# Optimization experiments

Hardware: AMD Instinct MI355X
Metric: run time of the kernel (lower is better)

## Reference

```python
import jax, jax.numpy as jnp
import numpy as np
import math

K = 3
IN_CH = 512
OUT_CH = 512
W_DIM = 512
B = 16
HW = 64
LR_MUL = 1.0


def setup_inputs() -> dict:
    key = jax.random.key(0)
    k1, k2, k3, k4 = jax.random.split(key, 4)
    x = jax.random.normal(k1, (B, HW, HW, IN_CH), dtype=jnp.float32)
    w_latents = jax.random.normal(k2, (B, W_DIM), dtype=jnp.float32)
    w = jax.random.normal(k3, (K, K, IN_CH, OUT_CH), dtype=jnp.float32)  # init_std = 1/lr_mul = 1
    b = jnp.zeros((OUT_CH,), dtype=jnp.float32)
    fc_w = jax.random.normal(k4, (W_DIM, IN_CH), dtype=jnp.float32)
    fc_b = jnp.zeros((IN_CH,), dtype=jnp.float32)
    return {"x": x, "w_latents": w_latents, "w": w, "b": b, "fc_w": fc_w, "fc_b": fc_b}


def reference(x, w_latents, w, b, fc_w, fc_b):
    # equalized-LR runtime coefficients (gain=1)
    conv_coef = LR_MUL / math.sqrt(K * K * IN_CH)
    fc_coef = LR_MUL / math.sqrt(W_DIM)

    batch, H, W_, Cin = x.shape
    x_nchw = jnp.transpose(x, (0, 3, 1, 2))  # [B, Cin, H, W]

    weight = w * conv_coef  # [k,k,in,out]
    # style modulation: fully_connected (no lrelu) + 1
    s = w_latents @ (fc_w * fc_coef) + fc_b * LR_MUL + 1.0  # [B, in]

    # per-sample modulated weights [B,k,k,in,out]
    ww = weight[None] * s[:, None, None, :, None]
    # demodulation
    d = jax.lax.rsqrt(jnp.sum(jnp.square(ww), axis=(1, 2, 3)) + 1e-8)  # [B, out]
    ww = ww * d[:, None, None, None, :]

    # fused_modconv: grouped conv with groups = batch
    x_g = x_nchw.reshape(1, batch * Cin, H, W_)
    w_g = jnp.transpose(ww, (1, 2, 3, 0, 4)).reshape(K, K, Cin, batch * OUT_CH)
    y = jax.lax.conv_general_dilated(
        x_g, w_g,
        window_strides=(1, 1),
        padding='SAME',
        dimension_numbers=('NCHW', 'HWIO', 'NCHW'),
        feature_group_count=batch,
    )  # [1, B*out, H, W]
    y = y.reshape(batch, OUT_CH, H, W_)
    y = jnp.transpose(y, (0, 2, 3, 1))  # NHWC
    y = y + (b * LR_MUL)
    return y
```

## Files before the change

kernel.cpp:

```cpp
#include <hip/hip_runtime.h>
#include <hip/hip_bf16.h>

#define IN_CH 512
#define OUT_CH 512
#define W_DIM 512
#define BATCH 16
#define HWDIM 64
#define PADW 66

static constexpr float CONV_COEF = 0.014731391274719739f;
static constexpr float FC_COEF   = 0.044194173824159216f;

typedef __bf16 bf16x8 __attribute__((ext_vector_type(8)));
typedef float  f32x4  __attribute__((ext_vector_type(4)));

typedef __attribute__((address_space(1))) void gvoid;
typedef __attribute__((address_space(3))) void lvoid;

__device__ __forceinline__ void async_cp16(const void* g, void* l) {
    __builtin_amdgcn_global_load_lds((gvoid*)g, (lvoid*)l, 16, 0, 0);
}

__device__ __forceinline__ ushort f2bf(float f) {
    union { float f; unsigned u; } un; un.f = f;
    unsigned u = un.u;
    return (ushort)((u + 0x7fffu + ((u >> 16) & 1u)) >> 16);
}

__global__ void k_halo(ushort* __restrict__ xs) {
    int b = blockIdx.y;
    int pidx = blockIdx.x * 4 + (threadIdx.x >> 6);
    int ch = threadIdx.x & 63;
    int h, w;
    if (pidx < 66)       { h = 0;          w = pidx; }
    else if (pidx < 132) { h = 65;         w = pidx - 66; }
    else if (pidx < 196) { h = pidx - 131; w = 0; }
    else                 { h = pidx - 195; w = 65; }
    size_t base = (((size_t)(b * PADW + h)) * PADW + w) * IN_CH + ch * 8;
    uint4 z = {0u, 0u, 0u, 0u};
    *(uint4*)(xs + base) = z;
}

__global__ void k_style(const float* __restrict__ wl, const float* __restrict__ fcw,
                        const float* __restrict__ fcb, float* __restrict__ s) {
    int b = blockIdx.x;
    int i = blockIdx.y * 128 + threadIdx.x;
    __shared__ float lw[W_DIM];
    for (int j = threadIdx.x; j < W_DIM; j += 128) lw[j] = wl[b * W_DIM + j];
    __syncthreads();
    float acc = 0.f;
#pragma unroll 8
    for (int j = 0; j < W_DIM; ++j) acc += lw[j] * fcw[(size_t)j * IN_CH + i];
    s[b * IN_CH + i] = acc * FC_COEF + fcb[i] + 1.0f;
}

__global__ void k_xs(const float* __restrict__ x, const float* __restrict__ s,
                     ushort* __restrict__ xs) {
    int t = blockIdx.x * blockDim.x + threadIdx.x;
    int pix = t >> 7;
    int c = (t & 127) << 2;
    int b = pix >> 12;
    int hw = pix & 4095;
    int h = hw >> 6, w = hw & 63;
    float4 xv = ((const float4*)x)[t];
    float4 sv = ((const float4*)(s + b * IN_CH))[t & 127];
    ushort4 o;
    o.x = f2bf(xv.x * sv.x);
    o.y = f2bf(xv.y * sv.y);
    o.z = f2bf(xv.z * sv.z);
    o.w = f2bf(xv.w * sv.w);
    size_t dst = (((size_t)(b * PADW + h + 1)) * PADW + (w + 1)) * IN_CH + c;
    *(ushort4*)(xs + dst) = o;
}

__global__ void k_wt(const float* __restrict__ w, ushort* __restrict__ wT) {
    __shared__ float tile[32][33];
    int kk = blockIdx.z;
    const float* src = w + (size_t)kk * IN_CH * OUT_CH;
    ushort* dst = wT + (size_t)kk * IN_CH * OUT_CH;
    int i0 = blockIdx.y * 32;
    int o0 = blockIdx.x * 32;
    int tx = threadIdx.x, ty = threadIdx.y;
#pragma unroll
    for (int rr = 0; rr < 32; rr += 8)
        tile[ty + rr][tx] = src[(size_t)(i0 + ty + rr) * OUT_CH + o0 + tx];
    __syncthreads();
#pragma unroll
    for (int rr = 0; rr < 32; rr += 8)
        dst[(size_t)(o0 + ty + rr) * IN_CH + i0 + tx] = f2bf(tile[tx][ty + rr]);
}

__global__ void k_a2(const float* __restrict__ w, float* __restrict__ a2) {
    int n = blockIdx.x * blockDim.x + threadIdx.x;
    float sum = 0.f;
#pragma unroll
    for (int kk = 0; kk < 9; ++kk) {
        float v = w[(size_t)kk * (IN_CH * OUT_CH) + n];
        sum += v * v;
    }
    a2[n] = sum;
}

__global__ void k_dmod(const float* __restrict__ s, const float* __restrict__ a2,
                       float* __restrict__ dmod) {
    int b = blockIdx.x;
    int o = blockIdx.y * 128 + threadIdx.x;
    __shared__ float s2[IN_CH];
    for (int i = threadIdx.x; i < IN_CH; i += 128) {
        float v = s[b * IN_CH + i];
        s2[i] = v * v;
    }
    __syncthreads();
    float acc = 0.f;
#pragma unroll 8
    for (int i = 0; i < IN_CH; ++i) acc += s2[i] * a2[(size_t)i * OUT_CH + o];
    dmod[b * OUT_CH + o] = rsqrtf(acc * CONV_COEF * CONV_COEF + 1e-8f);
}


__device__ __forceinline__ int aoff_of(int t) {
    int kk = t >> 3;
    int c0 = (t & 7) << 6;
    int kh = (kk >= 6) ? 2 : ((kk >= 3) ? 1 : 0);
    int kw = kk - kh * 3;
    return (kh * PADW + kw) * IN_CH + c0;
}

__device__ __forceinline__ int boff_of(int t) {
    int kk = t >> 3;
    int c0 = (t & 7) << 6;
    return kk * (IN_CH * OUT_CH) + c0;
}

__device__ __forceinline__ void bar() {
    asm volatile("" ::: "memory");
    __builtin_amdgcn_s_barrier();
    asm volatile("" ::: "memory");
}

#define MFMA16(AV, MH)                                                        \
    __builtin_amdgcn_s_setprio(1);                                            \
    _Pragma("unroll")                                                         \
    for (int i = 0; i < 4; ++i)                                               \
        _Pragma("unroll")                                                     \
        for (int j = 0; j < 4; ++j)                                           \
            acc[(MH)*4 + i][j] = __builtin_amdgcn_mfma_f32_16x16x32_bf16(     \
                AV[i], bv[j], acc[(MH)*4 + i][j], 0, 0, 0);                   \
    __builtin_amdgcn_s_setprio(0);

__device__ __forceinline__ void step4(
    const ushort* __restrict__ aBase, const ushort* __restrict__ bBase,
    int pc0, int pc1,
    const ushort* __restrict__ gA, const ushort* __restrict__ gB,
    ushort* __restrict__ dA, ushort* __restrict__ dB,
    bool doStage, f32x4 (&acc)[8][4])
{
    bf16x8 av[4], bv[4];

#pragma unroll
    for (int f = 0; f < 4; ++f) bv[f] = *(const bf16x8*)(bBase + f * 1024 + pc0);
#pragma unroll
    for (int f = 0; f < 4; ++f) av[f] = *(const bf16x8*)(aBase + f * 1024 + pc0);
    if (doStage) {
#pragma unroll
        for (int i = 0; i < 4; ++i)
            async_cp16(gA + i * (PADW * IN_CH), dA + i * 4096);
    }
    bar();
    MFMA16(av, 0)
    bar();

#pragma unroll
    for (int f = 0; f < 4; ++f) av[f] = *(const bf16x8*)(aBase + 4096 + f * 1024 + pc0);
    if (doStage) {
#pragma unroll
        for (int i = 0; i < 4; ++i)
            async_cp16(gB + i * (64 * IN_CH), dB + i * 4096);
    }
    bar();
    MFMA16(av, 1)
    bar();

#pragma unroll
    for (int f = 0; f < 4; ++f) bv[f] = *(const bf16x8*)(bBase + f * 1024 + pc1);
#pragma unroll
    for (int f = 0; f < 4; ++f) av[f] = *(const bf16x8*)(aBase + f * 1024 + pc1);
    bar();
    MFMA16(av, 0)
    bar();

#pragma unroll
    for (int f = 0; f < 4; ++f) av[f] = *(const bf16x8*)(aBase + 4096 + f * 1024 + pc1);
    bar();
    MFMA16(av, 1)
    asm volatile("s_waitcnt vmcnt(0)" ::: "memory");
    bar();
}

__global__ __launch_bounds__(512, 2) void k_conv(
    const ushort* __restrict__ xs, const ushort* __restrict__ wT,
    const float* __restrict__ dmod, const float* __restrict__ bias,
    float* __restrict__ out) {
    __shared__ __align__(16) ushort smem[4][16384];

    const int tid = threadIdx.x;
    const int wave = tid >> 6;
    const int lane = tid & 63;
    const int srow = tid >> 3;
    const int lc = (tid & 7) ^ (srow & 7);

    const int wg = (blockIdx.x & 7) * 64 + (blockIdx.x >> 3);
    const int nt = wg >> 8;
    const int mt = wg & 255;
    const int b  = mt >> 4;
    const int h0 = (mt & 15) << 2;
    const int n0 = nt << 8;

    const ushort* gA0 = xs + (((size_t)(b * PADW + h0)) * PADW + srow) * IN_CH + lc * 8;
    const ushort* gB0 = wT + ((size_t)(n0 + srow)) * IN_CH + lc * 8;

    ushort* dA[2] = { &smem[0][wave * 512], &smem[2][wave * 512] };
    ushort* dB[2] = { &smem[1][wave * 512], &smem[3][wave * 512] };

    const int rlane = lane & 15;
    const int q = lane >> 4;
    const int wm = wave >> 2;
    const int wn = wave & 3;
    const int pc0 = ((q + 0) ^ (rlane & 7)) * 8;
    const int pc1 = ((q + 4) ^ (rlane & 7)) * 8;

    const ushort* aBase[2] = {
        &smem[0][(wm * 128 + rlane) * 64],
        &smem[2][(wm * 128 + rlane) * 64],
    };
    const ushort* bBase[2] = {
        &smem[1][(wn * 64 + rlane) * 64],
        &smem[3][(wn * 64 + rlane) * 64],
    };

    f32x4 acc[8][4];
#pragma unroll
    for (int i = 0; i < 8; ++i)
#pragma unroll
        for (int j = 0; j < 4; ++j) {
            f32x4 z = {0.f, 0.f, 0.f, 0.f};
            acc[i][j] = z;
        }

#pragma unroll
    for (int i = 0; i < 4; ++i) {
        async_cp16(gA0 + aoff_of(0) + i * (PADW * IN_CH), dA[0] + i * 4096);
        async_cp16(gB0 + boff_of(0) + i * (64 * IN_CH), dB[0] + i * 4096);
    }
    asm volatile("s_waitcnt vmcnt(0)" ::: "memory");
    bar();

#pragma unroll 1
    for (int t = 0; t < 72; t += 2) {
        step4(aBase[0], bBase[0], pc0, pc1,
              gA0 + aoff_of(t + 1), gB0 + boff_of(t + 1),
              dA[1], dB[1], true, acc);
        step4(aBase[1], bBase[1], pc0, pc1,
              gA0 + aoff_of(t + 2), gB0 + boff_of(t + 2),
              dA[0], dB[0], (t + 2 < 72), acc);
    }

#pragma unroll
    for (int j = 0; j < 4; ++j) {
        const int n = n0 + wn * 64 + j * 16 + rlane;
        const float scale = dmod[b * OUT_CH + n] * CONV_COEF;
        const float bv2 = bias[n];
#pragma unroll
        for (int i = 0; i < 8; ++i) {
#pragma unroll
            for (int e = 0; e < 4; ++e) {
                const int m = wm * 128 + i * 16 + q * 4 + e;
                const int h = h0 + (m >> 6);
                const int w = m & 63;
                out[(((size_t)(b * HWDIM + h)) * HWDIM + w) * OUT_CH + n] =
                    acc[i][j][e] * scale + bv2;
            }
        }
    }
}

extern "C" void kernel_launch(void* const* d_in, const int* in_sizes, int n_in,
                              void* d_out, int out_size, void* d_ws, size_t ws_size,
                              hipStream_t stream) {
    const float* x    = (const float*)d_in[0];
    const float* wl   = (const float*)d_in[1];
    const float* w    = (const float*)d_in[2];
    const float* bias = (const float*)d_in[3];
    const float* fcw  = (const float*)d_in[4];
    const float* fcb  = (const float*)d_in[5];
    float* out = (float*)d_out;

    char* ws = (char*)d_ws;
    const size_t XS_BYTES = (size_t)BATCH * PADW * PADW * IN_CH * 2;
    const size_t WT_BYTES = (size_t)9 * IN_CH * OUT_CH * 2;
    ushort* xs   = (ushort*)ws;
    ushort* wT   = (ushort*)(ws + XS_BYTES);
    float*  s    = (float*)(ws + XS_BYTES + WT_BYTES);
    float*  dmod = s + BATCH * IN_CH;
    float*  a2   = dmod + BATCH * OUT_CH;

    k_halo<<<dim3(65, BATCH), 256, 0, stream>>>(xs);
    k_style<<<dim3(BATCH, 4), 128, 0, stream>>>(wl, fcw, fcb, s);
    k_xs<<<(BATCH * HWDIM * HWDIM * IN_CH / 4) / 256, 256, 0, stream>>>(x, s, xs);
    k_wt<<<dim3(16, 16, 9), dim3(32, 8), 0, stream>>>(w, wT);
    k_a2<<<(IN_CH * OUT_CH) / 256, 256, 0, stream>>>(w, a2);
    k_dmod<<<dim3(BATCH, 4), 128, 0, stream>>>(s, a2, dmod);
    k_conv<<<512, 512, 0, stream>>>(xs, wT, dmod, bias, out);
}
```

Measured before the change: 549.5 us.

## Switch conv to 32x32x16 MFMA and merge preprocessing kernels into two launches

```diff
diff --git a/kernel.cpp b/kernel.cpp
--- a/kernel.cpp
+++ b/kernel.cpp
@@ -12,7 +12,7 @@
 static constexpr float FC_COEF   = 0.044194173824159216f;
 
 typedef __bf16 bf16x8 __attribute__((ext_vector_type(8)));
-typedef float  f32x4  __attribute__((ext_vector_type(4)));
+typedef float  f32x16 __attribute__((ext_vector_type(16)));
 
 typedef __attribute__((address_space(1))) void gvoid;
 typedef __attribute__((address_space(3))) void lvoid;
@@ -27,94 +27,104 @@
     return (ushort)((u + 0x7fffu + ((u >> 16) & 1u)) >> 16);
 }
 
-__global__ void k_halo(ushort* __restrict__ xs) {
-    int b = blockIdx.y;
-    int pidx = blockIdx.x * 4 + (threadIdx.x >> 6);
-    int ch = threadIdx.x & 63;
-    int h, w;
-    if (pidx < 66)       { h = 0;          w = pidx; }
-    else if (pidx < 132) { h = 65;         w = pidx - 66; }
-    else if (pidx < 196) { h = pidx - 131; w = 0; }
-    else                 { h = pidx - 195; w = 65; }
-    size_t base = (((size_t)(b * PADW + h)) * PADW + w) * IN_CH + ch * 8;
-    uint4 z = {0u, 0u, 0u, 0u};
-    *(uint4*)(xs + base) = z;
-}
-
-__global__ void k_style(const float* __restrict__ wl, const float* __restrict__ fcw,
-                        const float* __restrict__ fcb, float* __restrict__ s) {
-    int b = blockIdx.x;
-    int i = blockIdx.y * 128 + threadIdx.x;
-    __shared__ float lw[W_DIM];
-    for (int j = threadIdx.x; j < W_DIM; j += 128) lw[j] = wl[b * W_DIM + j];
-    __syncthreads();
-    float acc = 0.f;
+__global__ __launch_bounds__(256) void k_pre1(
+    const float* __restrict__ wl, const float* __restrict__ fcw,
+    const float* __restrict__ fcb, float* __restrict__ s,
+    const float* __restrict__ w, float* __restrict__ a2,
+    ushort* __restrict__ xs, ushort* __restrict__ wT) {
+    const int tid = threadIdx.x;
+    const int blk = blockIdx.x;
+
+    if (blk < 32) {
+        __shared__ float lw[W_DIM];
+        int b = blk >> 1;
+        int i = (blk & 1) * 256 + tid;
+        for (int j = tid; j < W_DIM; j += 256) lw[j] = wl[b * W_DIM + j];
+        __syncthreads();
+        float acc = 0.f;
 #pragma unroll 8
-    for (int j = 0; j < W_DIM; ++j) acc += lw[j] * fcw[(size_t)j * IN_CH + i];
-    s[b * IN_CH + i] = acc * FC_COEF + fcb[i] + 1.0f;
-}
-
-__global__ void k_xs(const float* __restrict__ x, const float* __restrict__ s,
-                     ushort* __restrict__ xs) {
-    int t = blockIdx.x * blockDim.x + threadIdx.x;
-    int pix = t >> 7;
-    int c = (t & 127) << 2;
-    int b = pix >> 12;
-    int hw = pix & 4095;
-    int h = hw >> 6, w = hw & 63;
-    float4 xv = ((const float4*)x)[t];
-    float4 sv = ((const float4*)(s + b * IN_CH))[t & 127];
-    ushort4 o;
-    o.x = f2bf(xv.x * sv.x);
-    o.y = f2bf(xv.y * sv.y);
-    o.z = f2bf(xv.z * sv.z);
-    o.w = f2bf(xv.w * sv.w);
-    size_t dst = (((size_t)(b * PADW + h + 1)) * PADW + (w + 1)) * IN_CH + c;
-    *(ushort4*)(xs + dst) = o;
-}
-
-__global__ void k_wt(const float* __restrict__ w, ushort* __restrict__ wT) {
-    __shared__ float tile[32][33];
-    int kk = blockIdx.z;
-    const float* src = w + (size_t)kk * IN_CH * OUT_CH;
-    ushort* dst = wT + (size_t)kk * IN_CH * OUT_CH;
-    int i0 = blockIdx.y * 32;
-    int o0 = blockIdx.x * 32;
-    int tx = threadIdx.x, ty = threadIdx.y;
-#pragma unroll
-    for (int rr = 0; rr < 32; rr += 8)
-        tile[ty + rr][tx] = src[(size_t)(i0 + ty + rr) * OUT_CH + o0 + tx];
-    __syncthreads();
-#pragma unroll
-    for (int rr = 0; rr < 32; rr += 8)
-        dst[(size_t)(o0 + ty + rr) * IN_CH + i0 + tx] = f2bf(tile[tx][ty + rr]);
-}
-
-__global__ void k_a2(const float* __restrict__ w, float* __restrict__ a2) {
-    int n = blockIdx.x * blockDim.x + threadIdx.x;
-    float sum = 0.f;
-#pragma unroll
-    for (int kk = 0; kk < 9; ++kk) {
-        float v = w[(size_t)kk * (IN_CH * OUT_CH) + n];
-        sum += v * v;
-    }
-    a2[n] = sum;
-}
-
-__global__ void k_dmod(const float* __restrict__ s, const float* __restrict__ a2,
-                       float* __restrict__ dmod) {
-    int b = blockIdx.x;
-    int o = blockIdx.y * 128 + threadIdx.x;
-    __shared__ float s2[IN_CH];
-    for (int i = threadIdx.x; i < IN_CH; i += 128) {
-        float v = s[b * IN_CH + i];
-        s2[i] = v * v;
-    }
-    __syncthreads();
-    float acc = 0.f;
+        for (int j = 0; j < W_DIM; ++j) acc += lw[j] * fcw[(size_t)j * IN_CH + i];
+        s[b * IN_CH + i] = acc * FC_COEF + fcb[i] + 1.0f;
+    } else if (blk < 1056) {
+        int n = (blk - 32) * 256 + tid;
+        float sum = 0.f;
+#pragma unroll
+        for (int kk = 0; kk < 9; ++kk) {
+            float v = w[(size_t)kk * (IN_CH * OUT_CH) + n];
+            sum += v * v;
+        }
+        a2[n] = sum;
+    } else if (blk < 2096) {
+        int idx = blk - 1056;
+        int b = idx / 65;
+        int pidx = (idx % 65) * 4 + (tid >> 6);
+        int ch = tid & 63;
+        int h, wq;
+        if (pidx < 66)       { h = 0;          wq = pidx; }
+        else if (pidx < 132) { h = 65;         wq = pidx - 66; }
+        else if (pidx < 196) { h = pidx - 131; wq = 0; }
+        else                 { h = pidx - 195; wq = 65; }
+        size_t base = (((size_t)(b * PADW + h)) * PADW + wq) * IN_CH + ch * 8;
+        uint4 z = {0u, 0u, 0u, 0u};
+        *(uint4*)(xs + base) = z;
+    } else {
+        __shared__ float tile[32][33];
+        int idx = blk - 2096;
+        int kk = idx >> 8;
+        int rem = idx & 255;
+        int o0 = (rem & 15) * 32;
+        int i0 = (rem >> 4) * 32;
+        int tx = tid & 31, ty = tid >> 5;
+        const float* src = w + (size_t)kk * IN_CH * OUT_CH;
+        ushort* dst = wT + (size_t)kk * IN_CH * OUT_CH;
+#pragma unroll
+        for (int rr = 0; rr < 32; rr += 8)
+            tile[ty + rr][tx] = src[(size_t)(i0 + ty + rr) * OUT_CH + o0 + tx];
+        __syncthreads();
+#pragma unroll
+        for (int rr = 0; rr < 32; rr += 8)
+            dst[(size_t)(o0 + ty + rr) * IN_CH + i0 + tx] = f2bf(tile[tx][ty + rr]);
+    }
+}
+
+__global__ __launch_bounds__(256) void k_pre2(
+    const float* __restrict__ x, const float* __restrict__ s,
+    ushort* __restrict__ xs, const float* __restrict__ a2,
+    float* __restrict__ dmod) {
+    const int tid = threadIdx.x;
+    const int blk = blockIdx.x;
+
+    if (blk < 32768) {
+        int t = blk * 256 + tid;
+        int pix = t >> 7;
+        int c = (t & 127) << 2;
+        int b = pix >> 12;
+        int hw = pix & 4095;
+        int h = hw >> 6, wq = hw & 63;
+        float4 xv = ((const float4*)x)[t];
+        float4 sv = ((const float4*)(s + b * IN_CH))[t & 127];
+        ushort4 o;
+        o.x = f2bf(xv.x * sv.x);
+        o.y = f2bf(xv.y * sv.y);
+        o.z = f2bf(xv.z * sv.z);
+        o.w = f2bf(xv.w * sv.w);
+        size_t dst = (((size_t)(b * PADW + h + 1)) * PADW + (wq + 1)) * IN_CH + c;
+        *(ushort4*)(xs + dst) = o;
+    } else {
+        __shared__ float s2[IN_CH];
+        int sb = blk - 32768;
+        int b = sb >> 1;
+        int o = (sb & 1) * 256 + tid;
+        for (int i = tid; i < IN_CH; i += 256) {
+            float v = s[b * IN_CH + i];
+            s2[i] = v * v;
+        }
+        __syncthreads();
+        float acc = 0.f;
 #pragma unroll 8
-    for (int i = 0; i < IN_CH; ++i) acc += s2[i] * a2[(size_t)i * OUT_CH + o];
-    dmod[b * OUT_CH + o] = rsqrtf(acc * CONV_COEF * CONV_COEF + 1e-8f);
+        for (int i = 0; i < IN_CH; ++i) acc += s2[i] * a2[(size_t)i * OUT_CH + o];
+        dmod[b * OUT_CH + o] = rsqrtf(acc * CONV_COEF * CONV_COEF + 1e-8f);
+    }
 }
 
 
@@ -138,63 +148,43 @@
     asm volatile("" ::: "memory");
 }
 
-#define MFMA16(AV, MH)                                                        \
-    __builtin_amdgcn_s_setprio(1);                                            \
-    _Pragma("unroll")                                                         \
-    for (int i = 0; i < 4; ++i)                                               \
-        _Pragma("unroll")                                                     \
-        for (int j = 0; j < 4; ++j)                                           \
-            acc[(MH)*4 + i][j] = __builtin_amdgcn_mfma_f32_16x16x32_bf16(     \
-                AV[i], bv[j], acc[(MH)*4 + i][j], 0, 0, 0);                   \
-    __builtin_amdgcn_s_setprio(0);
-
-__device__ __forceinline__ void step4(
+__device__ __forceinline__ void step32(
     const ushort* __restrict__ aBase, const ushort* __restrict__ bBase,
-    int pc0, int pc1,
+    int q2, int lane7,
     const ushort* __restrict__ gA, const ushort* __restrict__ gB,
     ushort* __restrict__ dA, ushort* __restrict__ dB,
-    bool doStage, f32x4 (&acc)[8][4])
+    bool doStage, f32x16 (&acc)[4][2])
 {
-    bf16x8 av[4], bv[4];
-
-#pragma unroll
-    for (int f = 0; f < 4; ++f) bv[f] = *(const bf16x8*)(bBase + f * 1024 + pc0);
-#pragma unroll
-    for (int f = 0; f < 4; ++f) av[f] = *(const bf16x8*)(aBase + f * 1024 + pc0);
-    if (doStage) {
+#pragma unroll
+    for (int sl = 0; sl < 4; ++sl) {
+        const int pc = ((2 * sl + q2) ^ lane7) * 8;
+        bf16x8 av[4], bv[2];
+#pragma unroll
+        for (int j = 0; j < 2; ++j) bv[j] = *(const bf16x8*)(bBase + j * 2048 + pc);
+#pragma unroll
+        for (int i = 0; i < 4; ++i) av[i] = *(const bf16x8*)(aBase + i * 2048 + pc);
+        if (sl == 0 && doStage) {
+#pragma unroll
+            for (int i = 0; i < 4; ++i)
+                async_cp16(gA + i * (PADW * IN_CH), dA + i * 4096);
+        }
+        if (sl == 1 && doStage) {
+#pragma unroll
+            for (int i = 0; i < 4; ++i)
+                async_cp16(gB + i * (64 * IN_CH), dB + i * 4096);
+        }
+        bar();
+        __builtin_amdgcn_s_setprio(1);
 #pragma unroll
         for (int i = 0; i < 4; ++i)
-            async_cp16(gA + i * (PADW * IN_CH), dA + i * 4096);
-    }
-    bar();
-    MFMA16(av, 0)
-    bar();
-
-#pragma unroll
-    for (int f = 0; f < 4; ++f) av[f] = *(const bf16x8*)(aBase + 4096 + f * 1024 + pc0);
-    if (doStage) {
-#pragma unroll
-        for (int i = 0; i < 4; ++i)
-            async_cp16(gB + i * (64 * IN_CH), dB + i * 4096);
-    }
-    bar();
-    MFMA16(av, 1)
-    bar();
-
-#pragma unroll
-    for (int f = 0; f < 4; ++f) bv[f] = *(const bf16x8*)(bBase + f * 1024 + pc1);
-#pragma unroll
-    for (int f = 0; f < 4; ++f) av[f] = *(const bf16x8*)(aBase + f * 1024 + pc1);
-    bar();
-    MFMA16(av, 0)
-    bar();
-
-#pragma unroll
-    for (int f = 0; f < 4; ++f) av[f] = *(const bf16x8*)(aBase + 4096 + f * 1024 + pc1);
-    bar();
-    MFMA16(av, 1)
-    asm volatile("s_waitcnt vmcnt(0)" ::: "memory");
-    bar();
+#pragma unroll
+            for (int j = 0; j < 2; ++j)
+                acc[i][j] = __builtin_amdgcn_mfma_f32_32x32x16_bf16(
+                    av[i], bv[j], acc[i][j], 0, 0, 0);
+        __builtin_amdgcn_s_setprio(0);
+        if (sl == 3) asm volatile("s_waitcnt vmcnt(0)" ::: "memory");
+        bar();
+    }
 }
 
 __global__ __launch_bounds__(512, 2) void k_conv(
@@ -222,30 +212,28 @@
     ushort* dA[2] = { &smem[0][wave * 512], &smem[2][wave * 512] };
     ushort* dB[2] = { &smem[1][wave * 512], &smem[3][wave * 512] };
 
-    const int rlane = lane & 15;
-    const int q = lane >> 4;
+    const int lane31 = lane & 31;
+    const int q2 = lane >> 5;
+    const int lane7 = lane & 7;
     const int wm = wave >> 2;
     const int wn = wave & 3;
-    const int pc0 = ((q + 0) ^ (rlane & 7)) * 8;
-    const int pc1 = ((q + 4) ^ (rlane & 7)) * 8;
 
     const ushort* aBase[2] = {
-        &smem[0][(wm * 128 + rlane) * 64],
-        &smem[2][(wm * 128 + rlane) * 64],
+        &smem[0][(wm * 128 + lane31) * 64],
+        &smem[2][(wm * 128 + lane31) * 64],
     };
     const ushort* bBase[2] = {
-        &smem[1][(wn * 64 + rlane) * 64],
-        &smem[3][(wn * 64 + rlane) * 64],
+        &smem[1][(wn * 64 + lane31) * 64],
+        &smem[3][(wn * 64 + lane31) * 64],
     };
 
-    f32x4 acc[8][4];
-#pragma unroll
-    for (int i = 0; i < 8; ++i)
-#pragma unroll
-        for (int j = 0; j < 4; ++j) {
-            f32x4 z = {0.f, 0.f, 0.f, 0.f};
-            acc[i][j] = z;
-        }
+    f32x16 acc[4][2];
+#pragma unroll
+    for (int i = 0; i < 4; ++i)
+#pragma unroll
+        for (int j = 0; j < 2; ++j)
+#pragma unroll
+            for (int e = 0; e < 16; ++e) acc[i][j][e] = 0.f;
 
 #pragma unroll
     for (int i = 0; i < 4; ++i) {
@@ -257,28 +245,28 @@
 
 #pragma unroll 1
     for (int t = 0; t < 72; t += 2) {
-        step4(aBase[0], bBase[0], pc0, pc1,
-              gA0 + aoff_of(t + 1), gB0 + boff_of(t + 1),
-              dA[1], dB[1], true, acc);
-        step4(aBase[1], bBase[1], pc0, pc1,
-              gA0 + aoff_of(t + 2), gB0 + boff_of(t + 2),
-              dA[0], dB[0], (t + 2 < 72), acc);
-    }
-
-#pragma unroll
-    for (int j = 0; j < 4; ++j) {
-        const int n = n0 + wn * 64 + j * 16 + rlane;
+        step32(aBase[0], bBase[0], q2, lane7,
+               gA0 + aoff_of(t + 1), gB0 + boff_of(t + 1),
+               dA[1], dB[1], true, acc);
+        step32(aBase[1], bBase[1], q2, lane7,
+               gA0 + aoff_of(t + 2), gB0 + boff_of(t + 2),
+               dA[0], dB[0], (t + 2 < 72), acc);
+    }
+
+#pragma unroll
+    for (int j = 0; j < 2; ++j) {
+        const int n = n0 + wn * 64 + j * 32 + lane31;
         const float scale = dmod[b * OUT_CH + n] * CONV_COEF;
         const float bv2 = bias[n];
 #pragma unroll
-        for (int i = 0; i < 8; ++i) {
-#pragma unroll
-            for (int e = 0; e < 4; ++e) {
-                const int m = wm * 128 + i * 16 + q * 4 + e;
+        for (int i = 0; i < 4; ++i) {
+#pragma unroll
+            for (int r = 0; r < 16; ++r) {
+                const int m = wm * 128 + i * 32 + (r & 3) + 8 * (r >> 2) + 4 * q2;
                 const int h = h0 + (m >> 6);
-                const int w = m & 63;
-                out[(((size_t)(b * HWDIM + h)) * HWDIM + w) * OUT_CH + n] =
-                    acc[i][j][e] * scale + bv2;
+                const int wq = m & 63;
+                out[(((size_t)(b * HWDIM + h)) * HWDIM + wq) * OUT_CH + n] =
+                    acc[i][j][r] * scale + bv2;
             }
         }
     }
@@ -304,11 +292,7 @@
     float*  dmod = s + BATCH * IN_CH;
     float*  a2   = dmod + BATCH * OUT_CH;
 
-    k_halo<<<dim3(65, BATCH), 256, 0, stream>>>(xs);
-    k_style<<<dim3(BATCH, 4), 128, 0, stream>>>(wl, fcw, fcb, s);
-    k_xs<<<(BATCH * HWDIM * HWDIM * IN_CH / 4) / 256, 256, 0, stream>>>(x, s, xs);
-    k_wt<<<dim3(16, 16, 9), dim3(32, 8), 0, stream>>>(w, wT);
-    k_a2<<<(IN_CH * OUT_CH) / 256, 256, 0, stream>>>(w, a2);
-    k_dmod<<<dim3(BATCH, 4), 128, 0, stream>>>(s, a2, dmod);
+    k_pre1<<<4400, 256, 0, stream>>>(wl, fcw, fcb, s, w, a2, xs, wT);
+    k_pre2<<<32800, 256, 0, stream>>>(x, s, xs, a2, dmod);
     k_conv<<<512, 512, 0, stream>>>(xs, wT, dmod, bias, out);
 }
```

Result: slower. 572.0 us (+4.1%).
